# Kernel optimization log

Measured on AMD Instinct MI355X. Metric: run time of the kernel, lower is better.

## Reference

```python
import jax, jax.numpy as jnp
import numpy as np

N, E, R, F, HD = 4096, 2048, 4, 128, 256
DEG_EPS = 1e-8
BN_EPS = 1e-5
LN_EPS = 1e-5


def _xavier(k, shape):
    scale = np.sqrt(2.0 / (shape[-2] + shape[-1])).astype(np.float32)
    return jax.random.normal(k, shape, jnp.float32) * scale


def setup_inputs() -> dict:
    key = jax.random.key(0)
    ks = jax.random.split(key, 8)
    X = jax.random.normal(ks[0], (N, F), jnp.float32)
    # sparse binary incidence matrices, one per relation type, stacked [R,N,E]
    H = (jax.random.uniform(ks[1], (R, N, E)) < 0.05).astype(jnp.float32)
    return {
        "X": X,
        "H": H,
        "W1": _xavier(ks[2], (R, F, HD)),
        "W2": _xavier(ks[3], (R, HD, HD)),
        "W3": _xavier(ks[4], (R, HD, F)),
        "imp": jnp.ones((3, R), jnp.float32),        # relation_importance per conv layer
        "b1": jnp.zeros((HD,), jnp.float32),
        "b2": jnp.zeros((HD,), jnp.float32),
        "b3": jnp.zeros((F,), jnp.float32),
        "bn_gamma": jnp.ones((2, HD), jnp.float32),
        "bn_beta": jnp.zeros((2, HD), jnp.float32),
        "ln_gamma": jnp.ones((2, HD), jnp.float32),
        "ln_beta": jnp.zeros((2, HD), jnp.float32),
        "rel_attn": jnp.ones((R,), jnp.float32) / R,
    }


def typed_conv(X, Hw, W, imp, bias):
    # Hw: [R,N,E] weighted incidence; theta = Dv^{-1/2} H De^{-1/2} via row/col scaling
    dv = jnp.power(Hw.sum(axis=2) + DEG_EPS, -0.5)   # [R,N]
    de = jnp.power(Hw.sum(axis=1) + DEG_EPS, -0.5)   # [R,E]
    theta = Hw * dv[:, :, None] * de[:, None, :]     # [R,N,E]
    # (theta @ theta^T) @ X computed as theta @ (theta^T @ X) -- same math, no NxN
    t = jnp.einsum('rne,nf->ref', theta, X)          # [R,E,Fin]
    Hn = jnp.einsum('rne,ref->rnf', theta, t)        # [R,N,Fin]
    out = jnp.einsum('rnf,rfo->rno', Hn, W)          # [R,N,Fout]
    out = out * jax.nn.sigmoid(imp)[:, None, None]
    return out.sum(axis=0) + bias


def bn_ln_elu(X, bg, bb, lg, lb):
    # BatchNorm1d with batch statistics (biased var), then LayerNorm, then ELU
    mu = X.mean(axis=0)
    var = X.var(axis=0)
    X = (X - mu) * jax.lax.rsqrt(var + BN_EPS) * bg + bb
    m = X.mean(axis=-1, keepdims=True)
    v = X.var(axis=-1, keepdims=True)
    X = (X - m) * jax.lax.rsqrt(v + LN_EPS) * lg + lb
    return jax.nn.elu(X)


def reference(X, H, W1, W2, W3, imp, b1, b2, b3, bn_gamma, bn_beta, ln_gamma, ln_beta, rel_attn):
    rw = jax.nn.softmax(rel_attn)
    Hw = H * rw[:, None, None]                       # weighted incidence per relation
    h = typed_conv(X, Hw, W1, imp[0], b1)
    h = bn_ln_elu(h, bn_gamma[0], bn_beta[0], ln_gamma[0], ln_beta[0])
    h = typed_conv(h, Hw, W2, imp[1], b2)
    h = bn_ln_elu(h, bn_gamma[1], bn_beta[1], ln_gamma[1], ln_beta[1])
    out = typed_conv(h, Hw, W3, imp[2], b3)
    return out + X  # residual: out_channels == in_channels by construction
```

## Files before the change

### kernel.cpp

```cpp
#include <hip/hip_runtime.h>
#include <hip/hip_bf16.h>

#define NN 4096
#define EE 2048
#define RR 4
#define FF 128
#define HDD 256

typedef __attribute__((ext_vector_type(4))) float floatx4;
typedef __attribute__((ext_vector_type(8))) __bf16 bf16x8;

#define AS1 __attribute__((address_space(1)))
#define AS3 __attribute__((address_space(3)))

__device__ __forceinline__ void async16(const void* g, void* l) {
  __builtin_amdgcn_global_load_lds((const AS1 void*)(unsigned long long)(g),
                                   (AS3 void*)(unsigned int)(unsigned long long)(l),
                                   16, 0, 0);
}

__device__ inline unsigned short f2b(float x) {
  unsigned int u = __float_as_uint(x);
  unsigned int r = u + 0x7fffu + ((u >> 16) & 1u);
  return (unsigned short)(r >> 16);
}
__device__ inline float b2f(unsigned short u) { return __uint_as_float((unsigned int)u << 16); }

__device__ inline float rel_w(const float* rel, int r) {
  float m = fmaxf(fmaxf(rel[0], rel[1]), fmaxf(rel[2], rel[3]));
  float s = 0.f;
#pragma unroll
  for (int i = 0; i < RR; i++) s += expf(rel[i] - m);
  return expf(rel[r] - m) / s;
}

__global__ void k_dvmask(const float* __restrict__ H, const float* __restrict__ rel,
                         float* __restrict__ dvs, unsigned long long* __restrict__ mask) {
  int wave = (blockIdx.x << 2) | (threadIdx.x >> 6);
  int lane = threadIdx.x & 63;
  int r = wave >> 12;
  const float* row = H + (size_t)wave * EE;
  unsigned long long* mrow = mask + (size_t)wave * (EE / 64);
  float s = 0.f;
  for (int j = 0; j < EE / 64; j++) {
    float h = row[j * 64 + lane];
    s += h;
    unsigned long long m = __ballot(h != 0.0f);
    if (lane == 0) mrow[j] = m;
  }
  for (int off = 32; off; off >>= 1) s += __shfl_down(s, off);
  if (lane == 0) {
    float rwr = rel_w(rel, r);
    dvs[wave] = rwr * rsqrtf(rwr * s + 1e-8f);
  }
}

__global__ void k_de_pop(const unsigned long long* __restrict__ mask, float* __restrict__ de_acc) {
  int wid = threadIdx.x >> 6, lane = threadIdx.x & 63;
  int wcol = blockIdx.x, r = blockIdx.z;
  int n0 = (blockIdx.y << 8) + (wid << 6);
  unsigned long long w = mask[(size_t)(r * NN + n0 + lane) * (EE / 64) + wcol];
  float cnt = 0.f;
#pragma unroll
  for (int b = 0; b < 64; b++) {
    unsigned long long m = __ballot(((w >> b) & 1ULL) != 0);
    if (lane == b) cnt = (float)__popcll(m);
  }
  atomicAdd(&de_acc[r * EE + (wcol << 6) + lane], cnt);
}

__global__ void k_build_theta_bits(const unsigned long long* __restrict__ mask,
                                   const float* __restrict__ dvs, const float* __restrict__ decnt,
                                   const float* __restrict__ rel,
                                   unsigned short* __restrict__ theta, unsigned short* __restrict__ thetaT) {
  __shared__ unsigned short tile[64][65];
  int r = blockIdx.z;
  int e0 = blockIdx.x * 64, n0 = blockIdx.y * 64;
  int tr = threadIdx.x >> 4, tc = threadIdx.x & 15;
  float rwr = rel_w(rel, r);
  float de0 = rsqrtf(rwr * decnt[r * EE + e0 + tc * 4 + 0] + 1e-8f);
  float de1 = rsqrtf(rwr * decnt[r * EE + e0 + tc * 4 + 1] + 1e-8f);
  float de2 = rsqrtf(rwr * decnt[r * EE + e0 + tc * 4 + 2] + 1e-8f);
  float de3 = rsqrtf(rwr * decnt[r * EE + e0 + tc * 4 + 3] + 1e-8f);
  int wcol = e0 >> 6;
#pragma unroll
  for (int i = 0; i < 4; i++) {
    int n = n0 + tr + 16 * i;
    unsigned long long w = mask[((size_t)r * NN + n) * (EE / 64) + wcol];
    float d = dvs[r * NN + n];
    unsigned short b0 = ((w >> (tc * 4 + 0)) & 1) ? f2b(d * de0) : 0;
    unsigned short b1 = ((w >> (tc * 4 + 1)) & 1) ? f2b(d * de1) : 0;
    unsigned short b2 = ((w >> (tc * 4 + 2)) & 1) ? f2b(d * de2) : 0;
    unsigned short b3 = ((w >> (tc * 4 + 3)) & 1) ? f2b(d * de3) : 0;
    ushort4 o; o.x = b0; o.y = b1; o.z = b2; o.w = b3;
    *(ushort4*)(theta + ((size_t)r * NN + n) * EE + e0 + tc * 4) = o;
    tile[tr + 16 * i][tc * 4 + 0] = b0;
    tile[tr + 16 * i][tc * 4 + 1] = b1;
    tile[tr + 16 * i][tc * 4 + 2] = b2;
    tile[tr + 16 * i][tc * 4 + 3] = b3;
  }
  __syncthreads();
#pragma unroll
  for (int i = 0; i < 4; i++) {
    int e = e0 + tr + 16 * i;
    ushort4 o;
    o.x = tile[tc * 4 + 0][tr + 16 * i];
    o.y = tile[tc * 4 + 1][tr + 16 * i];
    o.z = tile[tc * 4 + 2][tr + 16 * i];
    o.w = tile[tc * 4 + 3][tr + 16 * i];
    *(ushort4*)(thetaT + ((size_t)r * EE + e) * NN + n0 + tc * 4) = o;
  }
}

__global__ void k_cvtT(const float* __restrict__ src, unsigned short* __restrict__ dst, int M, int C) {
  __shared__ unsigned short tile[64][65];
  int c0 = blockIdx.x * 64, m0 = blockIdx.y * 64;
  int tr = threadIdx.x >> 4, tc = threadIdx.x & 15;
#pragma unroll
  for (int i = 0; i < 4; i++) {
    int m = m0 + tr + 16 * i;
    float4 v = *(const float4*)(src + (size_t)m * C + c0 + tc * 4);
    tile[tr + 16 * i][tc * 4 + 0] = f2b(v.x);
    tile[tr + 16 * i][tc * 4 + 1] = f2b(v.y);
    tile[tr + 16 * i][tc * 4 + 2] = f2b(v.z);
    tile[tr + 16 * i][tc * 4 + 3] = f2b(v.w);
  }
  __syncthreads();
#pragma unroll
  for (int i = 0; i < 4; i++) {
    int c = c0 + tr + 16 * i;
    ushort4 v;
    v.x = tile[tc * 4 + 0][tr + 16 * i];
    v.y = tile[tc * 4 + 1][tr + 16 * i];
    v.z = tile[tc * 4 + 2][tr + 16 * i];
    v.w = tile[tc * 4 + 3][tr + 16 * i];
    *(ushort4*)(dst + (size_t)c * M + m0 + tc * 4) = v;
  }
}

__global__ void k_trz(const unsigned short* __restrict__ src, unsigned short* __restrict__ dst, int M, int C) {
  __shared__ unsigned short tile[64][65];
  int c0 = blockIdx.x * 64, m0 = blockIdx.y * 64;
  int tr = threadIdx.x >> 4, tc = threadIdx.x & 15;
#pragma unroll
  for (int i = 0; i < 4; i++) {
    int m = m0 + tr + 16 * i;
    ushort4 v = *(const ushort4*)(src + (size_t)m * C + c0 + tc * 4);
    tile[tr + 16 * i][tc * 4 + 0] = v.x;
    tile[tr + 16 * i][tc * 4 + 1] = v.y;
    tile[tr + 16 * i][tc * 4 + 2] = v.z;
    tile[tr + 16 * i][tc * 4 + 3] = v.w;
  }
  __syncthreads();
#pragma unroll
  for (int i = 0; i < 4; i++) {
    int c = c0 + tr + 16 * i;
    ushort4 v;
    v.x = tile[tc * 4 + 0][tr + 16 * i];
    v.y = tile[tc * 4 + 1][tr + 16 * i];
    v.z = tile[tc * 4 + 2][tr + 16 * i];
    v.w = tile[tc * 4 + 3][tr + 16 * i];
    *(ushort4*)(dst + (size_t)c * M + m0 + tc * 4) = v;
  }
}

__global__ void k_wprep(const float* __restrict__ W1, const float* __restrict__ W2,
                        const float* __restrict__ W3, const float* __restrict__ imp,
                        unsigned short* __restrict__ W1catT, unsigned short* __restrict__ W2T,
                        unsigned short* __restrict__ W3T) {
  int idx = blockIdx.x * 256 + threadIdx.x;
  if (idx < RR * FF * HDD) {
    int o = idx % HDD, f = (idx / HDD) % FF, r = idx / (HDD * FF);
    float sg = 1.0f / (1.0f + expf(-imp[r]));
    W1catT[(size_t)o * (RR * FF) + r * FF + f] = f2b(sg * W1[((size_t)r * FF + f) * HDD + o]);
  } else if (idx < RR * FF * HDD + RR * HDD * HDD) {
    int j = idx - RR * FF * HDD;
    int c = j % HDD, o = (j / HDD) % HDD, r = j / (HDD * HDD);
    float sg = 1.0f / (1.0f + expf(-imp[RR + r]));
    W2T[j] = f2b(sg * W2[((size_t)r * HDD + c) * HDD + o]);
  } else {
    int j = idx - RR * FF * HDD - RR * HDD * HDD;
    int c = j % HDD, o = (j / HDD) % FF, r = j / (HDD * FF);
    float sg = 1.0f / (1.0f + expf(-imp[2 * RR + r]));
    W3T[j] = f2b(sg * W3[((size_t)r * HDD + c) * FF + o]);
  }
}

__global__ __launch_bounds__(256) void k_gemm3(
    const unsigned short* __restrict__ A, const unsigned short* __restrict__ BT,
    int K, int SK, int lda, int ldb, long a_rs, long b_rs,
    unsigned short* __restrict__ P, long c_ps, int ldc) {
  __shared__ unsigned short Al[128 * 64];
  __shared__ unsigned short Bl[128 * 64];
  int tid = threadIdx.x, wid = tid >> 6, lane = tid & 63;
  int m0 = blockIdx.x << 7, n0 = blockIdx.y << 7;
  int z = blockIdx.z, zr = z / SK, kz = z - zr * SK;
  int Kc = K / SK;
  int r8 = lane >> 3, c8 = lane & 7;
  int swz = ((c8 ^ r8) << 3);
  const unsigned short* Ab = A + (size_t)zr * a_rs + (size_t)m0 * lda + (size_t)kz * Kc;
  const unsigned short* Bb = BT + (size_t)zr * b_rs + (size_t)n0 * ldb + (size_t)kz * Kc;
  int wm = (wid >> 1) << 6, wn = (wid & 1) << 6;
  int fm = lane & 15, quad = lane >> 4;
  int f7 = fm & 7;
  floatx4 acc[4][4];
#pragma unroll
  for (int i = 0; i < 4; i++)
#pragma unroll
    for (int j = 0; j < 4; j++) acc[i][j] = (floatx4){0.f, 0.f, 0.f, 0.f};
  for (int k0 = 0; k0 < Kc; k0 += 64) {
#pragma unroll
    for (int t = 0; t < 4; t++) {
      int rbase = (wid << 5) + (t << 3);
      int row = rbase + r8;
      async16(Ab + (size_t)row * lda + k0 + swz, &Al[rbase * 64 + lane * 8]);
      async16(Bb + (size_t)row * ldb + k0 + swz, &Bl[rbase * 64 + lane * 8]);
    }
    __syncthreads();
#pragma unroll
    for (int ks = 0; ks < 2; ks++) {
      int kg = (ks << 2) | quad;
      int ko = ((kg ^ f7) << 3);
      bf16x8 a[4], b[4];
#pragma unroll
      for (int i = 0; i < 4; i++) {
        a[i] = *(const bf16x8*)&Al[(wm + i * 16 + fm) * 64 + ko];
        b[i] = *(const bf16x8*)&Bl[(wn + i * 16 + fm) * 64 + ko];
      }
#pragma unroll
      for (int i = 0; i < 4; i++)
#pragma unroll
        for (int j = 0; j < 4; j++)
          acc[i][j] = __builtin_amdgcn_mfma_f32_16x16x32_bf16(a[i], b[j], acc[i][j], 0, 0, 0);
    }
    __syncthreads();
  }
  unsigned short* Cb = P + (size_t)z * c_ps;
#pragma unroll
  for (int mi = 0; mi < 4; mi++)
#pragma unroll
    for (int ni = 0; ni < 4; ni++)
#pragma unroll
      for (int v = 0; v < 4; v++) {
        int row = m0 + wm + mi * 16 + quad * 4 + v;
        int col = n0 + wn + ni * 16 + fm;
        Cb[(size_t)row * ldc + col] = f2b(acc[mi][ni][v]);
      }
}

__global__ void k_red_b(const unsigned short* __restrict__ P, unsigned short* __restrict__ out,
                        int SK, long region) {
  long i = ((long)blockIdx.x * 256 + threadIdx.x) * 8;
  int zr = blockIdx.y;
  const unsigned short* p = P + (size_t)zr * SK * region + i;
  float s[8] = {0, 0, 0, 0, 0, 0, 0, 0};
  for (int k = 0; k < SK; k++) {
    const unsigned short* q = p + (size_t)k * region;
    ushort4 a = *(const ushort4*)q;
    ushort4 b = *(const ushort4*)(q + 4);
    s[0] += b2f(a.x); s[1] += b2f(a.y); s[2] += b2f(a.z); s[3] += b2f(a.w);
    s[4] += b2f(b.x); s[5] += b2f(b.y); s[6] += b2f(b.z); s[7] += b2f(b.w);
  }
  ushort4 o0, o1;
  o0.x = f2b(s[0]); o0.y = f2b(s[1]); o0.z = f2b(s[2]); o0.w = f2b(s[3]);
  o1.x = f2b(s[4]); o1.y = f2b(s[5]); o1.z = f2b(s[6]); o1.w = f2b(s[7]);
  unsigned short* d = out + (size_t)zr * region + i;
  *(ushort4*)d = o0;
  *(ushort4*)(d + 4) = o1;
}

__global__ void k_red_hcatb(const unsigned short* __restrict__ P, unsigned short* __restrict__ out, int SK) {
  long i = ((long)blockIdx.x * 256 + threadIdx.x) * 8;
  int r = blockIdx.y;
  const unsigned short* p = P + (size_t)r * SK * (NN * FF) + i;
  float s[8] = {0, 0, 0, 0, 0, 0, 0, 0};
  for (int k = 0; k < SK; k++) {
    const unsigned short* q = p + (size_t)k * (NN * FF);
    ushort4 a = *(const ushort4*)q;
    ushort4 b = *(const ushort4*)(q + 4);
    s[0] += b2f(a.x); s[1] += b2f(a.y); s[2] += b2f(a.z); s[3] += b2f(a.w);
    s[4] += b2f(b.x); s[5] += b2f(b.y); s[6] += b2f(b.z); s[7] += b2f(b.w);
  }
  long n = i >> 7;
  int f = (int)(i & 127);
  ushort4 o0, o1;
  o0.x = f2b(s[0]); o0.y = f2b(s[1]); o0.z = f2b(s[2]); o0.w = f2b(s[3]);
  o1.x = f2b(s[4]); o1.y = f2b(s[5]); o1.z = f2b(s[6]); o1.w = f2b(s[7]);
  unsigned short* d = out + n * (RR * FF) + r * FF + f;
  *(ushort4*)d = o0;
  *(ushort4*)(d + 4) = o1;
}

__global__ void k_redstats(const unsigned short* __restrict__ P, float* __restrict__ out,
                           float* __restrict__ cs, float* __restrict__ cs2, int Z) {
  __shared__ float sm[2][8][256];
  int cg = (threadIdx.x & 31) << 3;
  int rowt = threadIdx.x >> 5;
  int r0 = blockIdx.x * 32;
  float s[8] = {0, 0, 0, 0, 0, 0, 0, 0}, s2[8] = {0, 0, 0, 0, 0, 0, 0, 0};
  for (int j = 0; j < 4; j++) {
    long idx = (long)(r0 + rowt * 4 + j) * HDD + cg;
    float acc[8] = {0, 0, 0, 0, 0, 0, 0, 0};
    for (int z = 0; z < Z; z++) {
      const unsigned short* p = P + (size_t)z * ((long)NN * HDD) + idx;
      ushort4 a = *(const ushort4*)p;
      ushort4 b = *(const ushort4*)(p + 4);
      acc[0] += b2f(a.x); acc[1] += b2f(a.y); acc[2] += b2f(a.z); acc[3] += b2f(a.w);
      acc[4] += b2f(b.x); acc[5] += b2f(b.y); acc[6] += b2f(b.z); acc[7] += b2f(b.w);
    }
    float4 o0 = {acc[0], acc[1], acc[2], acc[3]};
    float4 o1 = {acc[4], acc[5], acc[6], acc[7]};
    *(float4*)(out + idx) = o0;
    *(float4*)(out + idx + 4) = o1;
#pragma unroll
    for (int i = 0; i < 8; i++) { s[i] += acc[i]; s2[i] += acc[i] * acc[i]; }
  }
#pragma unroll
  for (int i = 0; i < 8; i++) { sm[0][rowt][cg + i] = s[i]; sm[1][rowt][cg + i] = s2[i]; }
  __syncthreads();
  int c = threadIdx.x;
  float a0 = 0, a1 = 0;
#pragma unroll
  for (int t = 0; t < 8; t++) { a0 += sm[0][t][c]; a1 += sm[1][t][c]; }
  atomicAdd(&cs[c], a0);
  atomicAdd(&cs2[c], a1);
}

__global__ void k_red_out(const unsigned short* __restrict__ P, const float* __restrict__ X,
                          const float* __restrict__ b3, float* __restrict__ out, int Z) {
  long i = ((long)blockIdx.x * 256 + threadIdx.x) * 4;
  int f = (int)(i & 127);
  float4 s = *(const float4*)(X + i);
  s.x += b3[f]; s.y += b3[f + 1]; s.z += b3[f + 2]; s.w += b3[f + 3];
  for (int z = 0; z < Z; z++) {
    ushort4 v = *(const ushort4*)(P + (size_t)z * (NN * FF) + i);
    s.x += b2f(v.x); s.y += b2f(v.y); s.z += b2f(v.z); s.w += b2f(v.w);
  }
  *(float4*)(out + i) = s;
}

__global__ void k_bnlnelu(const float* __restrict__ x, const float* __restrict__ cs, const float* __restrict__ cs2,
                          const float* __restrict__ bg, const float* __restrict__ bb,
                          const float* __restrict__ lg, const float* __restrict__ lb,
                          unsigned short* __restrict__ out) {
  int wid = threadIdx.x >> 6, lane = threadIdx.x & 63;
  int n = blockIdx.x * 4 + wid;
  float y[4];
  float m = 0.f;
#pragma unroll
  for (int j = 0; j < 4; j++) {
    int c = lane + 64 * j;
    float mu = cs[c] * (1.0f / NN);
    float var = cs2[c] * (1.0f / NN) - mu * mu;
    float xv = x[(size_t)n * HDD + c];
    y[j] = (xv - mu) * rsqrtf(var + 1e-5f) * bg[c] + bb[c];
    m += y[j];
  }
  for (int off = 32; off; off >>= 1) m += __shfl_down(m, off);
  m = __shfl(m, 0) * (1.0f / HDD);
  float var = 0.f;
#pragma unroll
  for (int j = 0; j < 4; j++) { float d = y[j] - m; var += d * d; }
  for (int off = 32; off; off >>= 1) var += __shfl_down(var, off);
  var = __shfl(var, 0) * (1.0f / HDD);
  float inv = rsqrtf(var + 1e-5f);
#pragma unroll
  for (int j = 0; j < 4; j++) {
    int c = lane + 64 * j;
    float z = (y[j] - m) * inv * lg[c] + lb[c];
    z = z > 0.f ? z : expm1f(z);
    out[(size_t)n * HDD + c] = f2b(z);
  }
}

extern "C" void kernel_launch(void* const* d_in, const int* in_sizes, int n_in,
                              void* d_out, int out_size, void* d_ws, size_t ws_size,
                              hipStream_t stream) {
  const float* X   = (const float*)d_in[0];
  const float* H   = (const float*)d_in[1];
  const float* W1  = (const float*)d_in[2];
  const float* W2  = (const float*)d_in[3];
  const float* W3  = (const float*)d_in[4];
  const float* imp = (const float*)d_in[5];
  const float* b3  = (const float*)d_in[8];
  const float* bng = (const float*)d_in[9];
  const float* bnb = (const float*)d_in[10];
  const float* lng = (const float*)d_in[11];
  const float* lnb = (const float*)d_in[12];
  const float* rel = (const float*)d_in[13];
  (void)in_sizes; (void)n_in; (void)out_size; (void)ws_size;

  char* w = (char*)d_ws;
  size_t off = 0;
  auto alloc = [&](size_t bytes) -> void* {
    void* p = w + off;
    off += (bytes + 255) & ~(size_t)255;
    return p;
  };
  float* dvs  = (float*)alloc((size_t)RR * NN * 4);
  float* de   = (float*)alloc((size_t)RR * EE * 4);
  float* cs   = (float*)alloc(2 * HDD * 4);
  unsigned long long* mask = (unsigned long long*)alloc((size_t)RR * NN * (EE / 64) * 8);
  unsigned short* theta  = (unsigned short*)alloc((size_t)RR * NN * EE * 2);
  unsigned short* thetaT = (unsigned short*)alloc((size_t)RR * NN * EE * 2);
  unsigned short* bufP = (unsigned short*)alloc((size_t)16 * NN * HDD * 2);
  unsigned short* bufC = (unsigned short*)alloc((size_t)RR * EE * HDD * 2);
  unsigned short* bufD = (unsigned short*)alloc((size_t)RR * EE * HDD * 2);
  unsigned short* bufE = (unsigned short*)alloc((size_t)RR * EE * HDD * 2);
  float* convout = (float*)alloc((size_t)NN * HDD * 4);
  unsigned short* Xb  = (unsigned short*)alloc((size_t)NN * HDD * 2);
  unsigned short* XbT = (unsigned short*)alloc((size_t)NN * HDD * 2);
  unsigned short* W1catT = (unsigned short*)alloc((size_t)RR * FF * HDD * 2);
  unsigned short* W2T    = (unsigned short*)alloc((size_t)RR * HDD * HDD * 2);
  unsigned short* W3T    = (unsigned short*)alloc((size_t)RR * HDD * FF * 2);

  k_dvmask<<<(RR * NN) / 4, 256, 0, stream>>>(H, rel, dvs, mask);
  hipMemsetAsync(de, 0, (size_t)RR * EE * 4, stream);
  k_de_pop<<<dim3(EE / 64, NN / 256, RR), 256, 0, stream>>>(mask, de);
  k_build_theta_bits<<<dim3(EE / 64, NN / 64, RR), 256, 0, stream>>>(mask, dvs, de, rel, theta, thetaT);
  k_cvtT<<<dim3(FF / 64, NN / 64), 256, 0, stream>>>(X, XbT, NN, FF);
  k_wprep<<<(RR * FF * HDD + RR * HDD * HDD + RR * HDD * FF) / 256, 256, 0, stream>>>(
      W1, W2, W3, imp, W1catT, W2T, W3T);

  k_gemm3<<<dim3(1, EE / 128, RR * 8), 256, 0, stream>>>(
      XbT, thetaT, NN, 8, NN, NN, 0, (long)EE * NN, bufP, (long)FF * EE, EE);
  k_red_b<<<dim3((FF * EE) / 2048, RR), 256, 0, stream>>>(bufP, bufC, 8, (long)FF * EE);
  k_gemm3<<<dim3(NN / 128, 1, RR * 2), 256, 0, stream>>>(
      theta, bufC, EE, 2, EE, EE, (long)NN * EE, (long)FF * EE, bufP, (long)NN * FF, FF);
  k_red_hcatb<<<dim3((NN * FF) / 2048, RR), 256, 0, stream>>>(bufP, bufD, 2);
  k_gemm3<<<dim3(NN / 128, HDD / 128, 4), 256, 0, stream>>>(
      bufD, W1catT, RR * FF, 4, RR * FF, RR * FF, 0, 0, bufP, (long)NN * HDD, HDD);
  hipMemsetAsync(cs, 0, 2 * HDD * 4, stream);
  k_redstats<<<NN / 32, 256, 0, stream>>>(bufP, convout, cs, cs + HDD, 4);
  k_bnlnelu<<<NN / 4, 256, 0, stream>>>(convout, cs, cs + HDD, bng, bnb, lng, lnb, Xb);
  k_trz<<<dim3(HDD / 64, NN / 64), 256, 0, stream>>>(Xb, XbT, NN, HDD);

  k_gemm3<<<dim3(64, HDD / 128, 4), 256, 0, stream>>>(
      thetaT, XbT, NN, 4, NN, NN, 0, 0, bufP, (long)RR * EE * HDD, HDD);
  k_red_b<<<dim3((RR * EE * HDD) / 2048, 1), 256, 0, stream>>>(bufP, bufD, 4, (long)RR * EE * HDD);
  k_gemm3<<<dim3(HDD / 128, EE / 128, RR), 256, 0, stream>>>(
      W2T, bufD, HDD, 1, HDD, HDD, (long)HDD * HDD, (long)EE * HDD, bufE, (long)HDD * EE, EE);
  k_gemm3<<<dim3(NN / 128, HDD / 128, RR * 2), 256, 0, stream>>>(
      theta, bufE, EE, 2, EE, EE, (long)NN * EE, (long)HDD * EE, bufP, (long)NN * HDD, HDD);
  hipMemsetAsync(cs, 0, 2 * HDD * 4, stream);
  k_redstats<<<NN / 32, 256, 0, stream>>>(bufP, convout, cs, cs + HDD, 8);
  k_bnlnelu<<<NN / 4, 256, 0, stream>>>(convout, cs, cs + HDD, bng + HDD, bnb + HDD, lng + HDD, lnb + HDD, Xb);

  k_gemm3<<<dim3(1, NN / 128, RR), 256, 0, stream>>>(
      W3T, Xb, HDD, 1, HDD, HDD, (long)FF * HDD, 0, bufD, (long)FF * NN, NN);
  k_gemm3<<<dim3(1, EE / 128, RR * 4), 256, 0, stream>>>(
      bufD, thetaT, NN, 4, NN, NN, (long)FF * NN, (long)EE * NN, bufP, (long)FF * EE, EE);
  k_red_b<<<dim3((FF * EE) / 2048, RR), 256, 0, stream>>>(bufP, bufC, 4, (long)FF * EE);
  k_gemm3<<<dim3(NN / 128, 1, RR * 2), 256, 0, stream>>>(
      theta, bufC, EE, 2, EE, EE, (long)NN * EE, (long)FF * EE, bufP, (long)NN * FF, FF);
  k_red_out<<<(NN * FF) / 1024, 256, 0, stream>>>(bufP, X, b3, (float*)d_out, 8);
}
```

Baseline: 488.0 us.

## Vectorize H scan with transposed mask layout and raise split-K across GEMMs

The incidence scan now reads float4 per lane and stores the bitmask word-major (transposed, interleaving edges by four), so mask writes and reads in the degree and theta-building kernels coalesce across nodes. Split-K factors are raised for several theta GEMMs to put more blocks on the GPU, with matching reduction counts. A swapxy flag reorders the block grid so neighbouring blocks share operand tiles. More split-K adds partial-sum traffic and reduction work.

```diff
diff --git a/kernel.cpp b/kernel.cpp
--- a/kernel.cpp
+++ b/kernel.cpp
@@ -39,14 +39,23 @@
   int wave = (blockIdx.x << 2) | (threadIdx.x >> 6);
   int lane = threadIdx.x & 63;
   int r = wave >> 12;
-  const float* row = H + (size_t)wave * EE;
-  unsigned long long* mrow = mask + (size_t)wave * (EE / 64);
+  int n = wave & (NN - 1);
+  const float4* row = (const float4*)(H + (size_t)wave * EE);
   float s = 0.f;
-  for (int j = 0; j < EE / 64; j++) {
-    float h = row[j * 64 + lane];
-    s += h;
-    unsigned long long m = __ballot(h != 0.0f);
-    if (lane == 0) mrow[j] = m;
+  for (int jj = 0; jj < 8; jj++) {
+    float4 v = row[jj * 64 + lane];
+    s += v.x + v.y + v.z + v.w;
+    unsigned long long m0 = __ballot(v.x != 0.0f);
+    unsigned long long m1 = __ballot(v.y != 0.0f);
+    unsigned long long m2 = __ballot(v.z != 0.0f);
+    unsigned long long m3 = __ballot(v.w != 0.0f);
+    if (lane == 0) {
+      size_t base = ((size_t)r * 32 + jj * 4) * NN + n;
+      mask[base] = m0;
+      mask[base + NN] = m1;
+      mask[base + 2 * NN] = m2;
+      mask[base + 3 * NN] = m3;
+    }
   }
   for (int off = 32; off; off >>= 1) s += __shfl_down(s, off);
   if (lane == 0) {
@@ -57,16 +66,17 @@
 
 __global__ void k_de_pop(const unsigned long long* __restrict__ mask, float* __restrict__ de_acc) {
   int wid = threadIdx.x >> 6, lane = threadIdx.x & 63;
-  int wcol = blockIdx.x, r = blockIdx.z;
+  int W = blockIdx.x, r = blockIdx.z;
   int n0 = (blockIdx.y << 8) + (wid << 6);
-  unsigned long long w = mask[(size_t)(r * NN + n0 + lane) * (EE / 64) + wcol];
+  unsigned long long w = mask[((size_t)r * 32 + W) * NN + n0 + lane];
   float cnt = 0.f;
 #pragma unroll
   for (int b = 0; b < 64; b++) {
     unsigned long long m = __ballot(((w >> b) & 1ULL) != 0);
     if (lane == b) cnt = (float)__popcll(m);
   }
-  atomicAdd(&de_acc[r * EE + (wcol << 6) + lane], cnt);
+  int e = ((W >> 2) << 8) + (lane << 2) + (W & 3);
+  atomicAdd(&de_acc[r * EE + e], cnt);
 }
 
 __global__ void k_build_theta_bits(const unsigned long long* __restrict__ mask,
@@ -75,23 +85,28 @@
                                    unsigned short* __restrict__ theta, unsigned short* __restrict__ thetaT) {
   __shared__ unsigned short tile[64][65];
   int r = blockIdx.z;
-  int e0 = blockIdx.x * 64, n0 = blockIdx.y * 64;
+  int bx = blockIdx.x;
+  int e0 = bx * 64, n0 = blockIdx.y * 64;
   int tr = threadIdx.x >> 4, tc = threadIdx.x & 15;
   float rwr = rel_w(rel, r);
   float de0 = rsqrtf(rwr * decnt[r * EE + e0 + tc * 4 + 0] + 1e-8f);
   float de1 = rsqrtf(rwr * decnt[r * EE + e0 + tc * 4 + 1] + 1e-8f);
   float de2 = rsqrtf(rwr * decnt[r * EE + e0 + tc * 4 + 2] + 1e-8f);
   float de3 = rsqrtf(rwr * decnt[r * EE + e0 + tc * 4 + 3] + 1e-8f);
-  int wcol = e0 >> 6;
+  size_t wbase = ((size_t)r * 32 + ((bx >> 2) << 2)) * NN;
+  int L = ((bx & 3) << 4) + tc;
 #pragma unroll
   for (int i = 0; i < 4; i++) {
     int n = n0 + tr + 16 * i;
-    unsigned long long w = mask[((size_t)r * NN + n) * (EE / 64) + wcol];
+    unsigned long long w0 = mask[wbase + n];
+    unsigned long long w1 = mask[wbase + NN + n];
+    unsigned long long w2 = mask[wbase + 2 * NN + n];
+    unsigned long long w3 = mask[wbase + 3 * NN + n];
     float d = dvs[r * NN + n];
-    unsigned short b0 = ((w >> (tc * 4 + 0)) & 1) ? f2b(d * de0) : 0;
-    unsigned short b1 = ((w >> (tc * 4 + 1)) & 1) ? f2b(d * de1) : 0;
-    unsigned short b2 = ((w >> (tc * 4 + 2)) & 1) ? f2b(d * de2) : 0;
-    unsigned short b3 = ((w >> (tc * 4 + 3)) & 1) ? f2b(d * de3) : 0;
+    unsigned short b0 = ((w0 >> L) & 1) ? f2b(d * de0) : 0;
+    unsigned short b1 = ((w1 >> L) & 1) ? f2b(d * de1) : 0;
+    unsigned short b2 = ((w2 >> L) & 1) ? f2b(d * de2) : 0;
+    unsigned short b3 = ((w3 >> L) & 1) ? f2b(d * de3) : 0;
     ushort4 o; o.x = b0; o.y = b1; o.z = b2; o.w = b3;
     *(ushort4*)(theta + ((size_t)r * NN + n) * EE + e0 + tc * 4) = o;
     tile[tr + 16 * i][tc * 4 + 0] = b0;
@@ -189,11 +204,12 @@
 __global__ __launch_bounds__(256) void k_gemm3(
     const unsigned short* __restrict__ A, const unsigned short* __restrict__ BT,
     int K, int SK, int lda, int ldb, long a_rs, long b_rs,
-    unsigned short* __restrict__ P, long c_ps, int ldc) {
+    unsigned short* __restrict__ P, long c_ps, int ldc, int swapxy) {
   __shared__ unsigned short Al[128 * 64];
   __shared__ unsigned short Bl[128 * 64];
   int tid = threadIdx.x, wid = tid >> 6, lane = tid & 63;
-  int m0 = blockIdx.x << 7, n0 = blockIdx.y << 7;
+  int bxx = blockIdx.x, byy = blockIdx.y;
+  int m0 = (swapxy ? byy : bxx) << 7, n0 = (swapxy ? bxx : byy) << 7;
   int z = blockIdx.z, zr = z / SK, kz = z - zr * SK;
   int Kc = K / SK;
   int r8 = lane >> 3, c8 = lane & 7;
@@ -423,35 +439,35 @@
       W1, W2, W3, imp, W1catT, W2T, W3T);
 
   k_gemm3<<<dim3(1, EE / 128, RR * 8), 256, 0, stream>>>(
-      XbT, thetaT, NN, 8, NN, NN, 0, (long)EE * NN, bufP, (long)FF * EE, EE);
+      XbT, thetaT, NN, 8, NN, NN, 0, (long)EE * NN, bufP, (long)FF * EE, EE, 0);
   k_red_b<<<dim3((FF * EE) / 2048, RR), 256, 0, stream>>>(bufP, bufC, 8, (long)FF * EE);
-  k_gemm3<<<dim3(NN / 128, 1, RR * 2), 256, 0, stream>>>(
-      theta, bufC, EE, 2, EE, EE, (long)NN * EE, (long)FF * EE, bufP, (long)NN * FF, FF);
-  k_red_hcatb<<<dim3((NN * FF) / 2048, RR), 256, 0, stream>>>(bufP, bufD, 2);
+  k_gemm3<<<dim3(NN / 128, 1, RR * 4), 256, 0, stream>>>(
+      theta, bufC, EE, 4, EE, EE, (long)NN * EE, (long)FF * EE, bufP, (long)NN * FF, FF, 0);
+  k_red_hcatb<<<dim3((NN * FF) / 2048, RR), 256, 0, stream>>>(bufP, bufD, 4);
   k_gemm3<<<dim3(NN / 128, HDD / 128, 4), 256, 0, stream>>>(
-      bufD, W1catT, RR * FF, 4, RR * FF, RR * FF, 0, 0, bufP, (long)NN * HDD, HDD);
+      bufD, W1catT, RR * FF, 4, RR * FF, RR * FF, 0, 0, bufP, (long)NN * HDD, HDD, 0);
   hipMemsetAsync(cs, 0, 2 * HDD * 4, stream);
   k_redstats<<<NN / 32, 256, 0, stream>>>(bufP, convout, cs, cs + HDD, 4);
   k_bnlnelu<<<NN / 4, 256, 0, stream>>>(convout, cs, cs + HDD, bng, bnb, lng, lnb, Xb);
   k_trz<<<dim3(HDD / 64, NN / 64), 256, 0, stream>>>(Xb, XbT, NN, HDD);
 
-  k_gemm3<<<dim3(64, HDD / 128, 4), 256, 0, stream>>>(
-      thetaT, XbT, NN, 4, NN, NN, 0, 0, bufP, (long)RR * EE * HDD, HDD);
-  k_red_b<<<dim3((RR * EE * HDD) / 2048, 1), 256, 0, stream>>>(bufP, bufD, 4, (long)RR * EE * HDD);
+  k_gemm3<<<dim3(2, 64, 8), 256, 0, stream>>>(
+      thetaT, XbT, NN, 8, NN, NN, 0, 0, bufP, (long)RR * EE * HDD, HDD, 1);
+  k_red_b<<<dim3((RR * EE * HDD) / 2048, 1), 256, 0, stream>>>(bufP, bufD, 8, (long)RR * EE * HDD);
   k_gemm3<<<dim3(HDD / 128, EE / 128, RR), 256, 0, stream>>>(
-      W2T, bufD, HDD, 1, HDD, HDD, (long)HDD * HDD, (long)EE * HDD, bufE, (long)HDD * EE, EE);
-  k_gemm3<<<dim3(NN / 128, HDD / 128, RR * 2), 256, 0, stream>>>(
-      theta, bufE, EE, 2, EE, EE, (long)NN * EE, (long)HDD * EE, bufP, (long)NN * HDD, HDD);
+      W2T, bufD, HDD, 1, HDD, HDD, (long)HDD * HDD, (long)EE * HDD, bufE, (long)HDD * EE, EE, 0);
+  k_gemm3<<<dim3(2, 32, RR * 4), 256, 0, stream>>>(
+      theta, bufE, EE, 4, EE, EE, (long)NN * EE, (long)HDD * EE, bufP, (long)NN * HDD, HDD, 1);
   hipMemsetAsync(cs, 0, 2 * HDD * 4, stream);
-  k_redstats<<<NN / 32, 256, 0, stream>>>(bufP, convout, cs, cs + HDD, 8);
+  k_redstats<<<NN / 32, 256, 0, stream>>>(bufP, convout, cs, cs + HDD, 16);
   k_bnlnelu<<<NN / 4, 256, 0, stream>>>(convout, cs, cs + HDD, bng + HDD, bnb + HDD, lng + HDD, lnb + HDD, Xb);
 
   k_gemm3<<<dim3(1, NN / 128, RR), 256, 0, stream>>>(
-      W3T, Xb, HDD, 1, HDD, HDD, (long)FF * HDD, 0, bufD, (long)FF * NN, NN);
-  k_gemm3<<<dim3(1, EE / 128, RR * 4), 256, 0, stream>>>(
-      bufD, thetaT, NN, 4, NN, NN, (long)FF * NN, (long)EE * NN, bufP, (long)FF * EE, EE);
-  k_red_b<<<dim3((FF * EE) / 2048, RR), 256, 0, stream>>>(bufP, bufC, 4, (long)FF * EE);
-  k_gemm3<<<dim3(NN / 128, 1, RR * 2), 256, 0, stream>>>(
-      theta, bufC, EE, 2, EE, EE, (long)NN * EE, (long)FF * EE, bufP, (long)NN * FF, FF);
-  k_red_out<<<(NN * FF) / 1024, 256, 0, stream>>>(bufP, X, b3, (float*)d_out, 8);
-}
+      W3T, Xb, HDD, 1, HDD, HDD, (long)FF * HDD, 0, bufD, (long)FF * NN, NN, 0);
+  k_gemm3<<<dim3(1, EE / 128, RR * 8), 256, 0, stream>>>(
+      bufD, thetaT, NN, 8, NN, NN, (long)FF * NN, (long)EE * NN, bufP, (long)FF * EE, EE, 0);
+  k_red_b<<<dim3((FF * EE) / 2048, RR), 256, 0, stream>>>(bufP, bufC, 8, (long)FF * EE);
+  k_gemm3<<<dim3(NN / 128, 1, RR * 4), 256, 0, stream>>>(
+      theta, bufC, EE, 4, EE, EE, (long)NN * EE, (long)FF * EE, bufP, (long)NN * FF, FF, 0);
+  k_red_out<<<(NN * FF) / 1024, 256, 0, stream>>>(bufP, X, b3, (float*)d_out, 16);
+}
```

Result: slower. 500.6 us (+2.6%).

## Decode theta on the fly from bitmasks inside GEMM instead of materializing bf16

Applied to the files above, without the earlier changes.

Removes the dense bf16 theta and thetaT matrices (4x4096x2048 each). The GEMM kernel instead rebuilds theta tiles in shared memory from packed incidence bitmasks and per-row and per-column degree scalings. A new mask-transpose kernel builds the transposed bitmask and the edge degree counts, and a small kernel precomputes the edge rsqrt factors. This cuts the large theta write/read memory traffic at the cost of ALU decode work and synchronous LDS stores in place of async loads inside the GEMM loop.

```diff
diff --git a/kernel.cpp b/kernel.cpp
--- a/kernel.cpp
+++ b/kernel.cpp
@@ -9,6 +9,7 @@
 
 typedef __attribute__((ext_vector_type(4))) float floatx4;
 typedef __attribute__((ext_vector_type(8))) __bf16 bf16x8;
+typedef __attribute__((ext_vector_type(8))) unsigned short ushort8;
 
 #define AS1 __attribute__((address_space(1)))
 #define AS3 __attribute__((address_space(3)))
@@ -55,61 +56,41 @@
   }
 }
 
-__global__ void k_de_pop(const unsigned long long* __restrict__ mask, float* __restrict__ de_acc) {
-  int wid = threadIdx.x >> 6, lane = threadIdx.x & 63;
-  int wcol = blockIdx.x, r = blockIdx.z;
-  int n0 = (blockIdx.y << 8) + (wid << 6);
-  unsigned long long w = mask[(size_t)(r * NN + n0 + lane) * (EE / 64) + wcol];
-  float cnt = 0.f;
-#pragma unroll
-  for (int b = 0; b < 64; b++) {
-    unsigned long long m = __ballot(((w >> b) & 1ULL) != 0);
-    if (lane == b) cnt = (float)__popcll(m);
-  }
-  atomicAdd(&de_acc[r * EE + (wcol << 6) + lane], cnt);
-}
-
-__global__ void k_build_theta_bits(const unsigned long long* __restrict__ mask,
-                                   const float* __restrict__ dvs, const float* __restrict__ decnt,
-                                   const float* __restrict__ rel,
-                                   unsigned short* __restrict__ theta, unsigned short* __restrict__ thetaT) {
-  __shared__ unsigned short tile[64][65];
-  int r = blockIdx.z;
-  int e0 = blockIdx.x * 64, n0 = blockIdx.y * 64;
-  int tr = threadIdx.x >> 4, tc = threadIdx.x & 15;
+__global__ void k_maskT(const unsigned long long* __restrict__ m1, unsigned long long* __restrict__ m2,
+                        float* __restrict__ de) {
+  __shared__ unsigned long long w[64 * 33];
+  int r = blockIdx.x >> 6;
+  int n0 = (blockIdx.x & 63) << 6;
+  int t = threadIdx.x;
+  const unsigned long long* src = m1 + ((size_t)r * NN + n0) * 32;
+#pragma unroll
+  for (int i = 0; i < 8; i++) {
+    int idx = t + i * 256;
+    int n = idx >> 5, W = idx & 31;
+    w[n * 33 + W] = src[idx];
+  }
+  __syncthreads();
+  int wid = t >> 6, lane = t & 63;
+  int v = n0 >> 6;
+#pragma unroll
+  for (int Wi = 0; Wi < 8; Wi++) {
+    int W = wid * 8 + Wi;
+    unsigned long long myw = w[lane * 33 + W];
+    unsigned long long out = 0;
+    for (int b = 0; b < 64; b++) {
+      unsigned long long mm = __ballot(((myw >> b) & 1ULL) != 0);
+      if (lane == b) out = mm;
+    }
+    m2[((size_t)r * EE + W * 64 + lane) * 64 + v] = out;
+    atomicAdd(&de[r * EE + W * 64 + lane], (float)__popcll(out));
+  }
+}
+
+__global__ void k_deR(const float* __restrict__ de, const float* __restrict__ rel, float* __restrict__ deR) {
+  int i = blockIdx.x * 256 + threadIdx.x;
+  int r = i >> 11;
   float rwr = rel_w(rel, r);
-  float de0 = rsqrtf(rwr * decnt[r * EE + e0 + tc * 4 + 0] + 1e-8f);
-  float de1 = rsqrtf(rwr * decnt[r * EE + e0 + tc * 4 + 1] + 1e-8f);
-  float de2 = rsqrtf(rwr * decnt[r * EE + e0 + tc * 4 + 2] + 1e-8f);
-  float de3 = rsqrtf(rwr * decnt[r * EE + e0 + tc * 4 + 3] + 1e-8f);
-  int wcol = e0 >> 6;
-#pragma unroll
-  for (int i = 0; i < 4; i++) {
-    int n = n0 + tr + 16 * i;
-    unsigned long long w = mask[((size_t)r * NN + n) * (EE / 64) + wcol];
-    float d = dvs[r * NN + n];
-    unsigned short b0 = ((w >> (tc * 4 + 0)) & 1) ? f2b(d * de0) : 0;
-    unsigned short b1 = ((w >> (tc * 4 + 1)) & 1) ? f2b(d * de1) : 0;
-    unsigned short b2 = ((w >> (tc * 4 + 2)) & 1) ? f2b(d * de2) : 0;
-    unsigned short b3 = ((w >> (tc * 4 + 3)) & 1) ? f2b(d * de3) : 0;
-    ushort4 o; o.x = b0; o.y = b1; o.z = b2; o.w = b3;
-    *(ushort4*)(theta + ((size_t)r * NN + n) * EE + e0 + tc * 4) = o;
-    tile[tr + 16 * i][tc * 4 + 0] = b0;
-    tile[tr + 16 * i][tc * 4 + 1] = b1;
-    tile[tr + 16 * i][tc * 4 + 2] = b2;
-    tile[tr + 16 * i][tc * 4 + 3] = b3;
-  }
-  __syncthreads();
-#pragma unroll
-  for (int i = 0; i < 4; i++) {
-    int e = e0 + tr + 16 * i;
-    ushort4 o;
-    o.x = tile[tc * 4 + 0][tr + 16 * i];
-    o.y = tile[tc * 4 + 1][tr + 16 * i];
-    o.z = tile[tc * 4 + 2][tr + 16 * i];
-    o.w = tile[tc * 4 + 3][tr + 16 * i];
-    *(ushort4*)(thetaT + ((size_t)r * EE + e) * NN + n0 + tc * 4) = o;
-  }
+  deR[i] = rsqrtf(rwr * de[i] + 1e-8f);
 }
 
 __global__ void k_cvtT(const float* __restrict__ src, unsigned short* __restrict__ dst, int M, int C) {
@@ -186,10 +167,13 @@
   }
 }
 
+template <int DECA, int DECB>
 __global__ __launch_bounds__(256) void k_gemm3(
     const unsigned short* __restrict__ A, const unsigned short* __restrict__ BT,
     int K, int SK, int lda, int ldb, long a_rs, long b_rs,
-    unsigned short* __restrict__ P, long c_ps, int ldc) {
+    unsigned short* __restrict__ P, long c_ps, long c_rs, int ldc,
+    const unsigned long long* __restrict__ dm, int dnw,
+    const float* __restrict__ dal, const float* __restrict__ dbe, long drow_rs, long dbe_rs) {
   __shared__ unsigned short Al[128 * 64];
   __shared__ unsigned short Bl[128 * 64];
   int tid = threadIdx.x, wid = tid >> 6, lane = tid & 63;
@@ -198,8 +182,15 @@
   int Kc = K / SK;
   int r8 = lane >> 3, c8 = lane & 7;
   int swz = ((c8 ^ r8) << 3);
-  const unsigned short* Ab = A + (size_t)zr * a_rs + (size_t)m0 * lda + (size_t)kz * Kc;
-  const unsigned short* Bb = BT + (size_t)zr * b_rs + (size_t)n0 * ldb + (size_t)kz * Kc;
+  const unsigned short* Ab = A + (DECA ? 0 : ((size_t)zr * a_rs + (size_t)m0 * lda + (size_t)kz * Kc));
+  const unsigned short* Bb = BT + (DECB ? 0 : ((size_t)zr * b_rs + (size_t)n0 * ldb + (size_t)kz * Kc));
+  int drow = tid >> 1, dhalf = tid & 1;
+  long rowOff = (long)zr * drow_rs + (DECA ? m0 : n0) + drow;
+  float dalpha = (DECA || DECB) ? dal[rowOff] : 0.f;
+  const float* dbeta = (DECA || DECB) ? (dbe + (long)zr * dbe_rs) : nullptr;
+  int dsw = drow & 7;
+  unsigned short* Dl = DECA ? Al : Bl;
+
   int wm = (wid >> 1) << 6, wn = (wid & 1) << 6;
   int fm = lane & 15, quad = lane >> 4;
   int f7 = fm & 7;
@@ -209,12 +200,44 @@
 #pragma unroll
     for (int j = 0; j < 4; j++) acc[i][j] = (floatx4){0.f, 0.f, 0.f, 0.f};
   for (int k0 = 0; k0 < Kc; k0 += 64) {
-#pragma unroll
-    for (int t = 0; t < 4; t++) {
-      int rbase = (wid << 5) + (t << 3);
-      int row = rbase + r8;
-      async16(Ab + (size_t)row * lda + k0 + swz, &Al[rbase * 64 + lane * 8]);
-      async16(Bb + (size_t)row * ldb + k0 + swz, &Bl[rbase * 64 + lane * 8]);
+    if (!DECA) {
+#pragma unroll
+      for (int t = 0; t < 4; t++) {
+        int rbase = (wid << 5) + (t << 3);
+        int row = rbase + r8;
+        async16(Ab + (size_t)row * lda + k0 + swz, &Al[rbase * 64 + lane * 8]);
+      }
+    }
+    if (!DECB) {
+#pragma unroll
+      for (int t = 0; t < 4; t++) {
+        int rbase = (wid << 5) + (t << 3);
+        int row = rbase + r8;
+        async16(Bb + (size_t)row * ldb + k0 + swz, &Bl[rbase * 64 + lane * 8]);
+      }
+    }
+    if (DECA || DECB) {
+      long kglob = (long)kz * Kc + k0;
+      const unsigned int* wp = (const unsigned int*)(dm + (size_t)rowOff * dnw + (kglob >> 6));
+      unsigned int bits = wp[dhalf];
+      const float* bp = dbeta + kglob + dhalf * 32;
+#pragma unroll
+      for (int g = 0; g < 4; g++) {
+        float4 p0 = *(const float4*)(bp + g * 8);
+        float4 p1 = *(const float4*)(bp + g * 8 + 4);
+        unsigned int bb = bits >> (g * 8);
+        ushort8 v;
+        v[0] = (bb & 1u)   ? f2b(dalpha * p0.x) : (unsigned short)0;
+        v[1] = (bb & 2u)   ? f2b(dalpha * p0.y) : (unsigned short)0;
+        v[2] = (bb & 4u)   ? f2b(dalpha * p0.z) : (unsigned short)0;
+        v[3] = (bb & 8u)   ? f2b(dalpha * p0.w) : (unsigned short)0;
+        v[4] = (bb & 16u)  ? f2b(dalpha * p1.x) : (unsigned short)0;
+        v[5] = (bb & 32u)  ? f2b(dalpha * p1.y) : (unsigned short)0;
+        v[6] = (bb & 64u)  ? f2b(dalpha * p1.z) : (unsigned short)0;
+        v[7] = (bb & 128u) ? f2b(dalpha * p1.w) : (unsigned short)0;
+        int chunk = ((dhalf << 2) | g) ^ dsw;
+        *(ushort8*)&Dl[drow * 64 + chunk * 8] = v;
+      }
     }
     __syncthreads();
 #pragma unroll
@@ -235,7 +258,7 @@
     }
     __syncthreads();
   }
-  unsigned short* Cb = P + (size_t)z * c_ps;
+  unsigned short* Cb = P + (size_t)kz * c_ps + (size_t)zr * c_rs;
 #pragma unroll
   for (int mi = 0; mi < 4; mi++)
 #pragma unroll
@@ -399,10 +422,10 @@
   };
   float* dvs  = (float*)alloc((size_t)RR * NN * 4);
   float* de   = (float*)alloc((size_t)RR * EE * 4);
+  float* deR  = (float*)alloc((size_t)RR * EE * 4);
   float* cs   = (float*)alloc(2 * HDD * 4);
-  unsigned long long* mask = (unsigned long long*)alloc((size_t)RR * NN * (EE / 64) * 8);
-  unsigned short* theta  = (unsigned short*)alloc((size_t)RR * NN * EE * 2);
-  unsigned short* thetaT = (unsigned short*)alloc((size_t)RR * NN * EE * 2);
+  unsigned long long* mask1 = (unsigned long long*)alloc((size_t)RR * NN * (EE / 64) * 8);
+  unsigned long long* mask2 = (unsigned long long*)alloc((size_t)RR * EE * (NN / 64) * 8);
   unsigned short* bufP = (unsigned short*)alloc((size_t)16 * NN * HDD * 2);
   unsigned short* bufC = (unsigned short*)alloc((size_t)RR * EE * HDD * 2);
   unsigned short* bufD = (unsigned short*)alloc((size_t)RR * EE * HDD * 2);
@@ -414,44 +437,53 @@
   unsigned short* W2T    = (unsigned short*)alloc((size_t)RR * HDD * HDD * 2);
   unsigned short* W3T    = (unsigned short*)alloc((size_t)RR * HDD * FF * 2);
 
-  k_dvmask<<<(RR * NN) / 4, 256, 0, stream>>>(H, rel, dvs, mask);
+  k_dvmask<<<(RR * NN) / 4, 256, 0, stream>>>(H, rel, dvs, mask1);
   hipMemsetAsync(de, 0, (size_t)RR * EE * 4, stream);
-  k_de_pop<<<dim3(EE / 64, NN / 256, RR), 256, 0, stream>>>(mask, de);
-  k_build_theta_bits<<<dim3(EE / 64, NN / 64, RR), 256, 0, stream>>>(mask, dvs, de, rel, theta, thetaT);
+  k_maskT<<<RR * (NN / 64), 256, 0, stream>>>(mask1, mask2, de);
+  k_deR<<<(RR * EE) / 256, 256, 0, stream>>>(de, rel, deR);
   k_cvtT<<<dim3(FF / 64, NN / 64), 256, 0, stream>>>(X, XbT, NN, FF);
   k_wprep<<<(RR * FF * HDD + RR * HDD * HDD + RR * HDD * FF) / 256, 256, 0, stream>>>(
       W1, W2, W3, imp, W1catT, W2T, W3T);
 
-  k_gemm3<<<dim3(1, EE / 128, RR * 8), 256, 0, stream>>>(
-      XbT, thetaT, NN, 8, NN, NN, 0, (long)EE * NN, bufP, (long)FF * EE, EE);
+  k_gemm3<0, 1><<<dim3(1, EE / 128, RR * 8), 256, 0, stream>>>(
+      XbT, nullptr, NN, 8, NN, 0, 0, 0, bufP, (long)FF * EE, 8L * FF * EE, EE,
+      mask2, NN / 64, deR, dvs, EE, NN);
   k_red_b<<<dim3((FF * EE) / 2048, RR), 256, 0, stream>>>(bufP, bufC, 8, (long)FF * EE);
-  k_gemm3<<<dim3(NN / 128, 1, RR * 2), 256, 0, stream>>>(
-      theta, bufC, EE, 2, EE, EE, (long)NN * EE, (long)FF * EE, bufP, (long)NN * FF, FF);
+  k_gemm3<1, 0><<<dim3(NN / 128, 1, RR * 2), 256, 0, stream>>>(
+      nullptr, bufC, EE, 2, 0, EE, 0, (long)FF * EE, bufP, (long)NN * FF, 2L * NN * FF, FF,
+      mask1, EE / 64, dvs, deR, NN, EE);
   k_red_hcatb<<<dim3((NN * FF) / 2048, RR), 256, 0, stream>>>(bufP, bufD, 2);
-  k_gemm3<<<dim3(NN / 128, HDD / 128, 4), 256, 0, stream>>>(
-      bufD, W1catT, RR * FF, 4, RR * FF, RR * FF, 0, 0, bufP, (long)NN * HDD, HDD);
+  k_gemm3<0, 0><<<dim3(NN / 128, HDD / 128, 4), 256, 0, stream>>>(
+      bufD, W1catT, RR * FF, 4, RR * FF, RR * FF, 0, 0, bufP, (long)NN * HDD, 4L * NN * HDD, HDD,
+      nullptr, 0, nullptr, nullptr, 0, 0);
   hipMemsetAsync(cs, 0, 2 * HDD * 4, stream);
   k_redstats<<<NN / 32, 256, 0, stream>>>(bufP, convout, cs, cs + HDD, 4);
   k_bnlnelu<<<NN / 4, 256, 0, stream>>>(convout, cs, cs + HDD, bng, bnb, lng, lnb, Xb);
   k_trz<<<dim3(HDD / 64, NN / 64), 256, 0, stream>>>(Xb, XbT, NN, HDD);
 
-  k_gemm3<<<dim3(64, HDD / 128, 4), 256, 0, stream>>>(
-      thetaT, XbT, NN, 4, NN, NN, 0, 0, bufP, (long)RR * EE * HDD, HDD);
+  k_gemm3<1, 0><<<dim3(EE / 128, HDD / 128, RR * 4), 256, 0, stream>>>(
+      nullptr, XbT, NN, 4, 0, NN, 0, 0, bufP, (long)RR * EE * HDD, (long)EE * HDD, HDD,
+      mask2, NN / 64, deR, dvs, EE, NN);
   k_red_b<<<dim3((RR * EE * HDD) / 2048, 1), 256, 0, stream>>>(bufP, bufD, 4, (long)RR * EE * HDD);
-  k_gemm3<<<dim3(HDD / 128, EE / 128, RR), 256, 0, stream>>>(
-      W2T, bufD, HDD, 1, HDD, HDD, (long)HDD * HDD, (long)EE * HDD, bufE, (long)HDD * EE, EE);
-  k_gemm3<<<dim3(NN / 128, HDD / 128, RR * 2), 256, 0, stream>>>(
-      theta, bufE, EE, 2, EE, EE, (long)NN * EE, (long)HDD * EE, bufP, (long)NN * HDD, HDD);
+  k_gemm3<0, 0><<<dim3(HDD / 128, EE / 128, RR), 256, 0, stream>>>(
+      W2T, bufD, HDD, 1, HDD, HDD, (long)HDD * HDD, (long)EE * HDD, bufE, (long)HDD * EE, (long)HDD * EE, EE,
+      nullptr, 0, nullptr, nullptr, 0, 0);
+  k_gemm3<1, 0><<<dim3(NN / 128, HDD / 128, RR * 2), 256, 0, stream>>>(
+      nullptr, bufE, EE, 2, 0, EE, 0, (long)HDD * EE, bufP, (long)NN * HDD, 2L * NN * HDD, HDD,
+      mask1, EE / 64, dvs, deR, NN, EE);
   hipMemsetAsync(cs, 0, 2 * HDD * 4, stream);
   k_redstats<<<NN / 32, 256, 0, stream>>>(bufP, convout, cs, cs + HDD, 8);
   k_bnlnelu<<<NN / 4, 256, 0, stream>>>(convout, cs, cs + HDD, bng + HDD, bnb + HDD, lng + HDD, lnb + HDD, Xb);
 
-  k_gemm3<<<dim3(1, NN / 128, RR), 256, 0, stream>>>(
-      W3T, Xb, HDD, 1, HDD, HDD, (long)FF * HDD, 0, bufD, (long)FF * NN, NN);
-  k_gemm3<<<dim3(1, EE / 128, RR * 4), 256, 0, stream>>>(
-      bufD, thetaT, NN, 4, NN, NN, (long)FF * NN, (long)EE * NN, bufP, (long)FF * EE, EE);
+  k_gemm3<0, 0><<<dim3(1, NN / 128, RR), 256, 0, stream>>>(
+      W3T, Xb, HDD, 1, HDD, HDD, (long)FF * HDD, 0, bufD, (long)FF * NN, (long)FF * NN, NN,
+      nullptr, 0, nullptr, nullptr, 0, 0);
+  k_gemm3<0, 1><<<dim3(1, EE / 128, RR * 4), 256, 0, stream>>>(
+      bufD, nullptr, NN, 4, NN, 0, (long)FF * NN, 0, bufP, (long)FF * EE, 4L * FF * EE, EE,
+      mask2, NN / 64, deR, dvs, EE, NN);
   k_red_b<<<dim3((FF * EE) / 2048, RR), 256, 0, stream>>>(bufP, bufC, 4, (long)FF * EE);
-  k_gemm3<<<dim3(NN / 128, 1, RR * 2), 256, 0, stream>>>(
-      theta, bufC, EE, 2, EE, EE, (long)NN * EE, (long)FF * EE, bufP, (long)NN * FF, FF);
+  k_gemm3<1, 0><<<dim3(NN / 128, 1, RR * 2), 256, 0, stream>>>(
+      nullptr, bufC, EE, 2, 0, EE, 0, (long)FF * EE, bufP, (long)NN * FF, 2L * NN * FF, FF,
+      mask1, EE / 64, dvs, deR, NN, EE);
   k_red_out<<<(NN * FF) / 1024, 256, 0, stream>>>(bufP, X, b3, (float*)d_out, 8);
 }
```

New measurement: 597.4 us. 22.4% more time.
